# Kernel tuning notes

Hardware: AMD Instinct MI355X
Metric: run time of the kernel (lower is better)

Reference implementation:

```python
import jax, jax.numpy as jnp
import numpy as np

N_NODES = 50000
N_EDGES = 600000
N_GRAPHS = 1024
H = 128
VOCAB = 32
NC = 2
BN_EPS = 1e-5


def setup_inputs() -> dict:
    key = jax.random.key(0)
    ks = jax.random.split(key, 16)
    rn = lambda k, s, sc=0.05: jax.random.normal(k, s, jnp.float32) * sc
    inp = {}
    inp["node_feat"] = jax.random.randint(ks[0], (N_NODES,), 0, VOCAB, dtype=jnp.int32)
    inp["edge_src"] = jax.random.randint(ks[1], (N_EDGES,), 0, N_NODES, dtype=jnp.int32)
    inp["edge_dst"] = jax.random.randint(ks[2], (N_EDGES,), 0, N_NODES, dtype=jnp.int32)
    inp["graph_ids"] = jnp.sort(jax.random.randint(ks[3], (N_NODES,), 0, N_GRAPHS, dtype=jnp.int32))
    inp["emb"] = rn(ks[4], (VOCAB, H))
    inp["W1"] = rn(ks[5], (H, H)); inp["b1"] = jnp.zeros((H,), jnp.float32)
    inp["W2"] = rn(ks[6], (H, H)); inp["b2"] = jnp.zeros((H,), jnp.float32)
    inp["e1_w"] = rn(ks[7], (H, H));   inp["e1_b"] = jnp.zeros((H,), jnp.float32)
    inp["e2_w"] = rn(ks[8], (H, H));   inp["e2_b"] = jnp.zeros((H,), jnp.float32)
    inp["e3_w"] = rn(ks[9], (H, 64));  inp["e3_b"] = jnp.zeros((64,), jnp.float32)
    inp["e4_w"] = rn(ks[10], (64, 32)); inp["e4_b"] = jnp.zeros((32,), jnp.float32)
    inp["e5_w"] = rn(ks[11], (32, NC)); inp["e5_b"] = jnp.zeros((NC,), jnp.float32)
    inp["bn0_g"] = jnp.ones((H,), jnp.float32); inp["bn0_b"] = jnp.zeros((H,), jnp.float32)
    inp["bn1_g"] = jnp.ones((H,), jnp.float32); inp["bn1_b"] = jnp.zeros((H,), jnp.float32)
    return inp


def reference(node_feat, edge_src, edge_dst, graph_ids,
              emb, W1, b1, W2, b2,
              e1_w, e1_b, e2_w, e2_b, e3_w, e3_b, e4_w, e4_b, e5_w, e5_b,
              bn0_g, bn0_b, bn1_g, bn1_b):
    ones_e = jnp.ones((N_EDGES,), jnp.float32)
    out_deg = jax.ops.segment_sum(ones_e, edge_src, num_segments=N_NODES)
    in_deg = jax.ops.segment_sum(ones_e, edge_dst, num_segments=N_NODES)
    # DGL GraphConv norm='both': D_out^{-1/2} pre-scale, D_in^{-1/2} post-scale (deg clamped to 1)
    oi = jax.lax.rsqrt(jnp.maximum(out_deg, 1.0))  # [N]
    ii = jax.lax.rsqrt(jnp.maximum(in_deg, 1.0))   # [N]

    def gconv(h, W, b):
        m = (h * oi[:, None])[edge_src]                                   # [E,H] gather
        agg = jax.ops.segment_sum(m, edge_dst, num_segments=N_NODES)      # [N,H] scatter-add
        return (agg * ii[:, None]) @ W + b

    h = emb[node_feat]                       # [N,H] embedding lookup
    h = jax.nn.relu(gconv(h, W1, b1))
    h = jax.nn.relu(gconv(h, W2, b2))

    # dgl.mean_nodes: per-graph mean over nodes
    cnt = jax.ops.segment_sum(jnp.ones((N_NODES,), jnp.float32), graph_ids, num_segments=N_GRAPHS)
    hg = jax.ops.segment_sum(h, graph_ids, num_segments=N_GRAPHS) / jnp.maximum(cnt, 1.0)[:, None]

    def bn(x, g, b):  # BatchNorm1d, training-mode batch stats (biased var)
        mu = x.mean(0)
        var = x.var(0)
        return (x - mu) * jax.lax.rsqrt(var + BN_EPS) * g + b

    def lrelu(x, s):
        return jnp.where(x >= 0, x, s * x)

    h1 = lrelu(bn(hg @ e1_w + e1_b, bn0_g, bn0_b), 0.05)
    h2 = lrelu(bn(h1 @ e2_w + e2_b, bn1_g, bn1_b), 0.05)
    h3 = lrelu(h2 @ e3_w + e3_b, 0.1)
    h4 = lrelu(h3 @ e4_w + e4_b, 0.1)
    y = h4 @ e5_w + e5_b                      # [G, NC]
    return jax.nn.log_softmax(y, axis=1)
```

## Files before the change

kernel.cpp:

```cpp
#include <hip/hip_runtime.h>
#include <hip/hip_bf16.h>
#include <math.h>

#define N_NODES 50000
#define N_PAD   50048
#define N_EDGES 600000
#define N_GRAPHS 1024
#define H 128
#define VOCAB 32
#define BN_EPS 1e-5f
#define SCAN_BLOCKS ((N_NODES + 255) / 256)
#define H1_NODES 64
#define EB ((N_EDGES + 255) / 256)

typedef short bf8_t __attribute__((ext_vector_type(8)));
typedef float f4_t __attribute__((ext_vector_type(4)));

__global__ void k_count_prep(const int* __restrict__ src, int* __restrict__ cntO,
                             const float* __restrict__ emb, const float* __restrict__ W1,
                             float* __restrict__ emb1,
                             const float* __restrict__ W2, __hip_bfloat16* __restrict__ w2t) {
    int b = blockIdx.x;
    int t = threadIdx.x;
    if (b < EB) {
        int i = b * 256 + t;
        if (i < N_EDGES) atomicAdd(&cntO[src[i]], 1);
    } else if (b < EB + 32) {
        if (t < 128) {
            int v = b - EB;
            float acc = 0.f;
            for (int k = 0; k < H; ++k) acc += emb[v * H + k] * W1[k * H + t];
            emb1[v * H + t] = acc;
        }
    } else {
        if (t < 128) {
            int k = b - EB - 32;
            w2t[(size_t)t * H + k] = __float2bfloat16(W2[(size_t)k * H + t]);
        }
    }
}

__global__ void k_hist64(const int* __restrict__ src, const int* __restrict__ dst,
                         const int* __restrict__ feat, const int* __restrict__ cntO,
                         unsigned long long* __restrict__ wc,
                         unsigned char* __restrict__ rank8, int E) {
    int i = blockIdx.x * blockDim.x + threadIdx.x;
    if (i >= E) return;
    int s = src[i], d = dst[i], v = feat[s];
    float o = rsqrtf(fmaxf((float)cntO[s], 1.f));
    unsigned long long q = (unsigned long long)__float2uint_rn(o * 16777216.0f);
    unsigned long long old = atomicAdd(&wc[(size_t)d * VOCAB + v], (1ULL << 40) | q);
    rank8[i] = (unsigned char)(old >> 40);
}

__global__ void k_nodebins(const unsigned long long* __restrict__ wc,
                           int* __restrict__ cntI, unsigned char* __restrict__ binbase,
                           int* __restrict__ bsum, int n) {
    __shared__ int scnt[256];
    int t = threadIdx.x;
    int wave = t >> 6, lane = t & 63;
    int sub = lane >> 5;
    int l32 = lane & 31;
    int nodeBase = blockIdx.x * 256;
#pragma unroll 4
    for (int it = 0; it < 32; ++it) {
        int local = wave * 64 + it * 2 + sub;
        int node = nodeBase + local;
        int c = 0;
        if (node < n && l32 < VOCAB)
            c = (int)(wc[(size_t)node * VOCAB + l32] >> 40);
        int inc = c;
#pragma unroll
        for (int off = 1; off < VOCAB; off <<= 1) {
            int u = __shfl_up(inc, off, 32);
            if (l32 >= off) inc += u;
        }
        if (node < n && l32 < VOCAB)
            binbase[(size_t)node * VOCAB + l32] = (unsigned char)(inc - c);
        if (l32 == VOCAB - 1) scnt[local] = (node < n) ? inc : 0;
    }
    __syncthreads();
    int node = nodeBase + t;
    if (node < n) cntI[node] = scnt[t];
    __shared__ int red[256];
    red[t] = scnt[t];
    __syncthreads();
    for (int off = 128; off > 0; off >>= 1) {
        if (t < off) red[t] += red[t + off];
        __syncthreads();
    }
    if (t == 0) bsum[blockIdx.x] = red[0];
}

__global__ void k_scanbsum(int* __restrict__ bsum, int* __restrict__ row_ptr_last, int nb) {
    __shared__ int sh[256];
    int t = threadIdx.x;
    int v = (t < nb) ? bsum[t] : 0;
    sh[t] = v;
    __syncthreads();
    for (int off = 1; off < 256; off <<= 1) {
        int u = (t >= off) ? sh[t - off] : 0;
        __syncthreads();
        sh[t] += u;
        __syncthreads();
    }
    if (t < nb) bsum[t] = sh[t] - v;
    if (t == nb - 1) *row_ptr_last = sh[t];
}

__global__ void k_scatterscan(const int* __restrict__ cntI, const int* __restrict__ bsum,
                              int* __restrict__ row_ptr, float* __restrict__ ii, int n) {
    __shared__ int sh[256];
    int i = blockIdx.x * 256 + threadIdx.x;
    int t = threadIdx.x;
    int v = (i < n) ? cntI[i] : 0;
    sh[t] = v;
    __syncthreads();
    for (int off = 1; off < 256; off <<= 1) {
        int u = (t >= off) ? sh[t - off] : 0;
        __syncthreads();
        sh[t] += u;
        __syncthreads();
    }
    if (i < n) {
        row_ptr[i] = bsum[blockIdx.x] + sh[t] - v;
        ii[i] = rsqrtf(fmaxf((float)v, 1.f));
    }
}

#define H1_BLOCKS ((N_NODES + H1_NODES - 1) / H1_NODES)
__global__ void k_fill_h1(const int* __restrict__ src, const int* __restrict__ dst,
                          const int* __restrict__ feat, const int* __restrict__ row_ptr,
                          const unsigned char* __restrict__ binbase,
                          const unsigned char* __restrict__ rank8,
                          int* __restrict__ col,
                          const unsigned long long* __restrict__ wc,
                          const float* __restrict__ emb1,
                          const float* __restrict__ ii, const int* __restrict__ cntO,
                          const float* __restrict__ b1, __hip_bfloat16* __restrict__ h1) {
    __shared__ float wl[H1_NODES * VOCAB];
    __shared__ float sii[H1_NODES], soi[H1_NODES];
    int tid = threadIdx.x;
    if (blockIdx.x < EB) {
        int i = blockIdx.x * 256 + tid;
        if (i < N_EDGES) {
            int s = src[i], d = dst[i], v = feat[s];
            int slot = row_ptr[d] + (int)binbase[(size_t)d * VOCAB + v] + (int)rank8[i];
            col[slot] = s;
        }
        return;
    }
    int hb = blockIdx.x - EB;
    int j = tid & 127;
    int g = tid >> 7;
    float ev[VOCAB];
#pragma unroll
    for (int v = 0; v < VOCAB; ++v) ev[v] = emb1[v * H + j];
    float bj = b1[j];

    int node0 = hb * H1_NODES;
    int nn = min(H1_NODES, N_NODES - node0);
    const unsigned long long* wsrc = wc + (size_t)node0 * VOCAB;
    for (int i = tid; i < nn * VOCAB; i += 256) {
        unsigned long long p = wsrc[i];
        float lo = (float)((unsigned)p & 0xFFFFFFu);
        float hi = (float)((unsigned)(p >> 24) & 0xFFFFu);
        wl[i] = fmaf(lo, 1.0f / 16777216.0f, hi);
    }
    for (int i = tid; i < nn; i += 256) {
        sii[i] = ii[node0 + i];
        soi[i] = rsqrtf(fmaxf((float)cntO[node0 + i], 1.f));
    }
    __syncthreads();

    int rbeg = g * 32;
    int rend = min(rbeg + 32, nn);
    for (int r = rbeg; r < rend; ++r) {
        const float4* wr = (const float4*)(wl + r * VOCAB);
        float acc = 0.f;
#pragma unroll
        for (int q = 0; q < VOCAB / 4; ++q) {
            float4 w4 = wr[q];
            acc += w4.x * ev[4 * q] + w4.y * ev[4 * q + 1]
                 + w4.z * ev[4 * q + 2] + w4.w * ev[4 * q + 3];
        }
        float val = fmaxf(acc * sii[r] + bj, 0.f);
        h1[(size_t)(node0 + r) * H + j] = __float2bfloat16(val * soi[r]);
    }
}

__global__ void k_gather_bf(const __hip_bfloat16* __restrict__ h,
                            const int* __restrict__ row_ptr, const int* __restrict__ col,
                            __hip_bfloat16* __restrict__ out, int n) {
    int gid = blockIdx.x * blockDim.x + threadIdx.x;
    int wid = gid >> 6;
    int lane = gid & 63;
    int node = wid * 2 + (lane >> 5);
    int l32 = lane & 31;
    if (node >= n) return;
    int beg = row_ptr[node];
    int end = row_ptr[node + 1];
    int co = l32 * 4;
    float a0 = 0.f, a1 = 0.f, a2 = 0.f, a3 = 0.f;
    int e = beg;
    for (; e + 8 <= end; e += 8) {
#pragma unroll
        for (int k = 0; k < 8; ++k) {
            int s = col[e + k];
            uint2 v = *(const uint2*)(h + (size_t)s * H + co);
            float2 f0 = __bfloat1622float2(*(__hip_bfloat162*)&v.x);
            float2 f1 = __bfloat1622float2(*(__hip_bfloat162*)&v.y);
            a0 += f0.x; a1 += f0.y; a2 += f1.x; a3 += f1.y;
        }
    }
    for (; e < end; ++e) {
        int s = col[e];
        uint2 v = *(const uint2*)(h + (size_t)s * H + co);
        float2 f0 = __bfloat1622float2(*(__hip_bfloat162*)&v.x);
        float2 f1 = __bfloat1622float2(*(__hip_bfloat162*)&v.y);
        a0 += f0.x; a1 += f0.y; a2 += f1.x; a3 += f1.y;
    }
    __hip_bfloat162 o0 = __float22bfloat162_rn(make_float2(a0, a1));
    __hip_bfloat162 o1 = __float22bfloat162_rn(make_float2(a2, a3));
    uint2 ov;
    ov.x = *(unsigned*)&o0;
    ov.y = *(unsigned*)&o1;
    *(uint2*)(out + (size_t)node * H + co) = ov;
}

__global__ void k_transform_mfma(const __hip_bfloat16* __restrict__ A,
                                 const __hip_bfloat16* __restrict__ WT,
                                 const float* __restrict__ ii,
                                 const float* __restrict__ b,
                                 float* __restrict__ outp, int n) {
    int wave = threadIdx.x >> 6;
    int lane = threadIdx.x & 63;
    int row0 = blockIdx.x * 64 + wave * 16;
    int rl = lane & 15;
    int kg = lane >> 4;
    f4_t acc[8];
#pragma unroll
    for (int t = 0; t < 8; ++t) acc[t] = f4_t{0.f, 0.f, 0.f, 0.f};
    const __hip_bfloat16* arow = A + (size_t)(row0 + rl) * H + kg * 8;
#pragma unroll
    for (int ks = 0; ks < 4; ++ks) {
        bf8_t a = *(const bf8_t*)(arow + ks * 32);
#pragma unroll
        for (int t = 0; t < 8; ++t) {
            bf8_t bf = *(const bf8_t*)(WT + (size_t)(t * 16 + rl) * H + ks * 32 + kg * 8);
            acc[t] = __builtin_amdgcn_mfma_f32_16x16x32_bf16(a, bf, acc[t], 0, 0, 0);
        }
    }
    int rbase = row0 + kg * 4;
#pragma unroll
    for (int r = 0; r < 4; ++r) {
        int node = rbase + r;
        if (node < n) {
            float s = ii[node];
#pragma unroll
            for (int t = 0; t < 8; ++t) {
                int c = t * 16 + rl;
                float v = acc[t][r] * s + b[c];
                outp[(size_t)node * H + c] = fmaxf(v, 0.f);
            }
        }
    }
}

__global__ void k_poolmlp1(const float* __restrict__ h, const int* __restrict__ gid,
                           const float* __restrict__ e1w, const float* __restrict__ e1b,
                           float* __restrict__ t1, int n) {
    __shared__ int bnd[2];
    __shared__ float row[128];
    int g = blockIdx.x, t = threadIdx.x;
    if (t == 0) {
        int lo = 0, hi = n;
        while (lo < hi) { int m = (lo + hi) >> 1; if (gid[m] < g) lo = m + 1; else hi = m; }
        bnd[0] = lo;
        int lo2 = lo, hi2 = n;
        while (lo2 < hi2) { int m = (lo2 + hi2) >> 1; if (gid[m] < g + 1) lo2 = m + 1; else hi2 = m; }
        bnd[1] = lo2;
    }
    __syncthreads();
    int beg = bnd[0], end = bnd[1];
    float s = 0.f;
    for (int i = beg; i < end; ++i) s += h[(size_t)i * H + t];
    row[t] = s / fmaxf((float)(end - beg), 1.f);
    __syncthreads();
    float acc = e1b[t];
    for (int k = 0; k < H; ++k) acc += row[k] * e1w[k * H + t];
    t1[g * H + t] = acc;
}

__global__ void k_bnstat(const float* __restrict__ x, float* __restrict__ stats, int G) {
    int c = blockIdx.x;
    float s = 0.f, s2 = 0.f;
    for (int g = threadIdx.x; g < G; g += blockDim.x) {
        float v = x[g * H + c];
        s += v; s2 += v * v;
    }
    __shared__ float rs[256], rs2[256];
    rs[threadIdx.x] = s; rs2[threadIdx.x] = s2;
    __syncthreads();
    for (int off = 128; off > 0; off >>= 1) {
        if (threadIdx.x < off) { rs[threadIdx.x] += rs[threadIdx.x + off]; rs2[threadIdx.x] += rs2[threadIdx.x + off]; }
        __syncthreads();
    }
    if (threadIdx.x == 0) {
        float mu = rs[0] / G;
        stats[c] = mu;
        stats[H + c] = rs2[0] / G - mu * mu;
    }
}

__global__ void k_mlp2bn(const float* __restrict__ t1, const float* __restrict__ stats,
                         const float* __restrict__ gam, const float* __restrict__ bet,
                         const float* __restrict__ W, const float* __restrict__ bias,
                         float* __restrict__ t2) {
    __shared__ float x[128];
    int g = blockIdx.x, t = threadIdx.x;
    float v = t1[g * H + t];
    v = (v - stats[t]) * rsqrtf(stats[H + t] + BN_EPS) * gam[t] + bet[t];
    x[t] = (v >= 0.f) ? v : 0.05f * v;
    __syncthreads();
    float acc = bias[t];
    for (int k = 0; k < H; ++k) acc += x[k] * W[k * H + t];
    t2[g * H + t] = acc;
}

__global__ void k_head(const float* __restrict__ t2, const float* __restrict__ stats,
                       const float* __restrict__ gam, const float* __restrict__ bet,
                       const float* __restrict__ e3w, const float* __restrict__ e3b,
                       const float* __restrict__ e4w, const float* __restrict__ e4b,
                       const float* __restrict__ e5w, const float* __restrict__ e5b,
                       float* __restrict__ out) {
    __shared__ float x[128], h3[64], h4[32];
    int g = blockIdx.x, t = threadIdx.x;
    float v = t2[g * H + t];
    v = (v - stats[t]) * rsqrtf(stats[H + t] + BN_EPS) * gam[t] + bet[t];
    x[t] = (v >= 0.f) ? v : 0.05f * v;
    __syncthreads();
    if (t < 64) {
        float a = e3b[t];
        for (int k = 0; k < 128; ++k) a += x[k] * e3w[k * 64 + t];
        h3[t] = (a >= 0.f) ? a : 0.1f * a;
    }
    __syncthreads();
    if (t < 32) {
        float a = e4b[t];
        for (int k = 0; k < 64; ++k) a += h3[k] * e4w[k * 32 + t];
        h4[t] = (a >= 0.f) ? a : 0.1f * a;
    }
    __syncthreads();
    if (t == 0) {
        float y0 = e5b[0], y1 = e5b[1];
        for (int k = 0; k < 32; ++k) {
            y0 += h4[k] * e5w[2 * k];
            y1 += h4[k] * e5w[2 * k + 1];
        }
        float m = fmaxf(y0, y1);
        float l = m + logf(expf(y0 - m) + expf(y1 - m));
        out[2 * g] = y0 - l;
        out[2 * g + 1] = y1 - l;
    }
}

extern "C" void kernel_launch(void* const* d_in, const int* in_sizes, int n_in,
                              void* d_out, int out_size, void* d_ws, size_t ws_size,
                              hipStream_t stream) {
    const int*   node_feat = (const int*)d_in[0];
    const int*   edge_src  = (const int*)d_in[1];
    const int*   edge_dst  = (const int*)d_in[2];
    const int*   graph_ids = (const int*)d_in[3];
    const float* emb  = (const float*)d_in[4];
    const float* W1   = (const float*)d_in[5];
    const float* b1   = (const float*)d_in[6];
    const float* W2   = (const float*)d_in[7];
    const float* b2   = (const float*)d_in[8];
    const float* e1_w = (const float*)d_in[9];
    const float* e1_b = (const float*)d_in[10];
    const float* e2_w = (const float*)d_in[11];
    const float* e2_b = (const float*)d_in[12];
    const float* e3_w = (const float*)d_in[13];
    const float* e3_b = (const float*)d_in[14];
    const float* e4_w = (const float*)d_in[15];
    const float* e4_b = (const float*)d_in[16];
    const float* e5_w = (const float*)d_in[17];
    const float* e5_b = (const float*)d_in[18];
    const float* bn0_g = (const float*)d_in[19];
    const float* bn0_b = (const float*)d_in[20];
    const float* bn1_g = (const float*)d_in[21];
    const float* bn1_b = (const float*)d_in[22];
    float* out = (float*)d_out;

    float* ws = (float*)d_ws;
    float* bufA = ws;
    __hip_bfloat16* h1bf = (__hip_bfloat16*)(bufA + (size_t)N_NODES * H);
    __hip_bfloat16* aggbf = h1bf + (size_t)N_NODES * H;
    int*   cntO = (int*)(aggbf + (size_t)N_PAD * H);
    unsigned long long* wc = (unsigned long long*)(cntO + N_NODES);
    float* ii   = (float*)(wc + (size_t)N_NODES * VOCAB);
    int*   cntI = (int*)(ii + N_NODES);
    int*   row_ptr = cntI + N_NODES;
    int*   col  = row_ptr + 50048;
    unsigned char* binbase = (unsigned char*)(col + N_EDGES);
    unsigned char* rank8   = binbase + (size_t)N_NODES * VOCAB;
    float* t1   = (float*)(rank8 + ((N_EDGES + 63) & ~63));
    float* t2   = t1 + N_GRAPHS * H;
    float* stats = t2 + N_GRAPHS * H;
    int*   bsum  = (int*)(stats + 4 * H);
    float* emb1  = (float*)(bsum + 256);
    __hip_bfloat16* w2t = (__hip_bfloat16*)(emb1 + VOCAB * H);

    hipMemsetAsync(cntO, 0, N_NODES * sizeof(int) + (size_t)N_NODES * VOCAB * 8, stream);

    k_count_prep<<<EB + 160, 256, 0, stream>>>(edge_src, cntO, emb, W1, emb1, W2, w2t);
    k_hist64<<<EB, 256, 0, stream>>>(edge_src, edge_dst, node_feat, cntO, wc, rank8, N_EDGES);
    k_nodebins<<<SCAN_BLOCKS, 256, 0, stream>>>(wc, cntI, binbase, bsum, N_NODES);
    k_scanbsum<<<1, 256, 0, stream>>>(bsum, row_ptr + N_NODES, SCAN_BLOCKS);
    k_scatterscan<<<SCAN_BLOCKS, 256, 0, stream>>>(cntI, bsum, row_ptr, ii, N_NODES);
    k_fill_h1<<<EB + H1_BLOCKS, 256, 0, stream>>>(edge_src, edge_dst, node_feat, row_ptr,
                                                  binbase, rank8, col,
                                                  wc, emb1, ii, cntO, b1, h1bf);

    const int gb = ((N_NODES + 1) / 2 * 64 + 255) / 256;
    k_gather_bf<<<gb, 256, 0, stream>>>(h1bf, row_ptr, col, aggbf, N_NODES);
    k_transform_mfma<<<(N_NODES + 63) / 64, 256, 0, stream>>>(aggbf, w2t, ii, b2, bufA, N_NODES);

    k_poolmlp1<<<N_GRAPHS, 128, 0, stream>>>(bufA, graph_ids, e1_w, e1_b, t1, N_NODES);
    k_bnstat<<<H, 256, 0, stream>>>(t1, stats, N_GRAPHS);
    k_mlp2bn<<<N_GRAPHS, 128, 0, stream>>>(t1, stats, bn0_g, bn0_b, e2_w, e2_b, t2);
    k_bnstat<<<H, 256, 0, stream>>>(t2, stats + 2 * H, N_GRAPHS);
    k_head<<<N_GRAPHS, 128, 0, stream>>>(t2, stats + 2 * H, bn1_g, bn1_b,
                                         e3_w, e3_b, e4_w, e4_b, e5_w, e5_b, out);
}
```

Measured before the change: 220.6 us.

## Merge edge histogram into count kernel, compute layer-1 via CSR gather

The separate 64-bit weighted histogram kernel is dropped. Per-(dst,vocab) counts now use 32-bit atomics inside the out-degree counting kernel, and the two-level scan is folded into one kernel so a launch is saved. Layer-1 aggregation is now a per-node CSR gather over emb1 rows instead of a histogram-times-embedding product, and the layer-2 gather uses 16 lanes per node with 16-byte loads. In exchange, layer 1 now does a full per-edge gather with indirect feat/cntO loads instead of a 32-wide dot product, and it runs one small block per node, which may cost more than the histogram path.

```diff
diff --git a/kernel.cpp b/kernel.cpp
--- a/kernel.cpp
+++ b/kernel.cpp
@@ -10,21 +10,28 @@
 #define VOCAB 32
 #define BN_EPS 1e-5f
 #define SCAN_BLOCKS ((N_NODES + 255) / 256)
-#define H1_NODES 64
 #define EB ((N_EDGES + 255) / 256)
 
 typedef short bf8_t __attribute__((ext_vector_type(8)));
 typedef float f4_t __attribute__((ext_vector_type(4)));
 
-__global__ void k_count_prep(const int* __restrict__ src, int* __restrict__ cntO,
-                             const float* __restrict__ emb, const float* __restrict__ W1,
-                             float* __restrict__ emb1,
-                             const float* __restrict__ W2, __hip_bfloat16* __restrict__ w2t) {
+__global__ void k_edge(const int* __restrict__ src, const int* __restrict__ dst,
+                       const int* __restrict__ feat,
+                       int* __restrict__ cntO, unsigned* __restrict__ cnt32,
+                       unsigned char* __restrict__ rank8,
+                       const float* __restrict__ emb, const float* __restrict__ W1,
+                       float* __restrict__ emb1,
+                       const float* __restrict__ W2, __hip_bfloat16* __restrict__ w2t) {
     int b = blockIdx.x;
     int t = threadIdx.x;
     if (b < EB) {
         int i = b * 256 + t;
-        if (i < N_EDGES) atomicAdd(&cntO[src[i]], 1);
+        if (i < N_EDGES) {
+            int s = src[i];
+            atomicAdd(&cntO[s], 1);
+            unsigned old = atomicAdd(&cnt32[(size_t)dst[i] * VOCAB + feat[s]], 1u);
+            rank8[i] = (unsigned char)old;
+        }
     } else if (b < EB + 32) {
         if (t < 128) {
             int v = b - EB;
@@ -40,20 +47,7 @@
     }
 }
 
-__global__ void k_hist64(const int* __restrict__ src, const int* __restrict__ dst,
-                         const int* __restrict__ feat, const int* __restrict__ cntO,
-                         unsigned long long* __restrict__ wc,
-                         unsigned char* __restrict__ rank8, int E) {
-    int i = blockIdx.x * blockDim.x + threadIdx.x;
-    if (i >= E) return;
-    int s = src[i], d = dst[i], v = feat[s];
-    float o = rsqrtf(fmaxf((float)cntO[s], 1.f));
-    unsigned long long q = (unsigned long long)__float2uint_rn(o * 16777216.0f);
-    unsigned long long old = atomicAdd(&wc[(size_t)d * VOCAB + v], (1ULL << 40) | q);
-    rank8[i] = (unsigned char)(old >> 40);
-}
-
-__global__ void k_nodebins(const unsigned long long* __restrict__ wc,
+__global__ void k_nodebins(const unsigned* __restrict__ cnt32,
                            int* __restrict__ cntI, unsigned char* __restrict__ binbase,
                            int* __restrict__ bsum, int n) {
     __shared__ int scnt[256];
@@ -68,7 +62,7 @@
         int node = nodeBase + local;
         int c = 0;
         if (node < n && l32 < VOCAB)
-            c = (int)(wc[(size_t)node * VOCAB + l32] >> 40);
+            c = (int)cnt32[(size_t)node * VOCAB + l32];
         int inc = c;
 #pragma unroll
         for (int off = 1; off < VOCAB; off <<= 1) {
@@ -92,10 +86,24 @@
     if (t == 0) bsum[blockIdx.x] = red[0];
 }
 
-__global__ void k_scanbsum(int* __restrict__ bsum, int* __restrict__ row_ptr_last, int nb) {
+__global__ void k_scatterscan(const int* __restrict__ cntI, const int* __restrict__ bsum,
+                              int* __restrict__ row_ptr, float* __restrict__ ii,
+                              int n, int nb) {
+    __shared__ int sb[256];
     __shared__ int sh[256];
     int t = threadIdx.x;
-    int v = (t < nb) ? bsum[t] : 0;
+    int bv = (t < nb) ? bsum[t] : 0;
+    sb[t] = bv;
+    __syncthreads();
+    for (int off = 1; off < 256; off <<= 1) {
+        int u = (t >= off) ? sb[t - off] : 0;
+        __syncthreads();
+        sb[t] += u;
+        __syncthreads();
+    }
+    int blockoff = (blockIdx.x == 0) ? 0 : sb[blockIdx.x - 1];
+    int i = blockIdx.x * 256 + t;
+    int v = (i < n) ? cntI[i] : 0;
     sh[t] = v;
     __syncthreads();
     for (int off = 1; off < 256; off <<= 1) {
@@ -104,89 +112,42 @@
         sh[t] += u;
         __syncthreads();
     }
-    if (t < nb) bsum[t] = sh[t] - v;
-    if (t == nb - 1) *row_ptr_last = sh[t];
-}
-
-__global__ void k_scatterscan(const int* __restrict__ cntI, const int* __restrict__ bsum,
-                              int* __restrict__ row_ptr, float* __restrict__ ii, int n) {
-    __shared__ int sh[256];
-    int i = blockIdx.x * 256 + threadIdx.x;
-    int t = threadIdx.x;
-    int v = (i < n) ? cntI[i] : 0;
-    sh[t] = v;
-    __syncthreads();
-    for (int off = 1; off < 256; off <<= 1) {
-        int u = (t >= off) ? sh[t - off] : 0;
-        __syncthreads();
-        sh[t] += u;
-        __syncthreads();
-    }
     if (i < n) {
-        row_ptr[i] = bsum[blockIdx.x] + sh[t] - v;
+        row_ptr[i] = blockoff + sh[t] - v;
         ii[i] = rsqrtf(fmaxf((float)v, 1.f));
     }
-}
-
-#define H1_BLOCKS ((N_NODES + H1_NODES - 1) / H1_NODES)
-__global__ void k_fill_h1(const int* __restrict__ src, const int* __restrict__ dst,
-                          const int* __restrict__ feat, const int* __restrict__ row_ptr,
-                          const unsigned char* __restrict__ binbase,
-                          const unsigned char* __restrict__ rank8,
-                          int* __restrict__ col,
-                          const unsigned long long* __restrict__ wc,
-                          const float* __restrict__ emb1,
-                          const float* __restrict__ ii, const int* __restrict__ cntO,
-                          const float* __restrict__ b1, __hip_bfloat16* __restrict__ h1) {
-    __shared__ float wl[H1_NODES * VOCAB];
-    __shared__ float sii[H1_NODES], soi[H1_NODES];
-    int tid = threadIdx.x;
-    if (blockIdx.x < EB) {
-        int i = blockIdx.x * 256 + tid;
-        if (i < N_EDGES) {
-            int s = src[i], d = dst[i], v = feat[s];
-            int slot = row_ptr[d] + (int)binbase[(size_t)d * VOCAB + v] + (int)rank8[i];
-            col[slot] = s;
-        }
-        return;
-    }
-    int hb = blockIdx.x - EB;
-    int j = tid & 127;
-    int g = tid >> 7;
-    float ev[VOCAB];
-#pragma unroll
-    for (int v = 0; v < VOCAB; ++v) ev[v] = emb1[v * H + j];
-    float bj = b1[j];
-
-    int node0 = hb * H1_NODES;
-    int nn = min(H1_NODES, N_NODES - node0);
-    const unsigned long long* wsrc = wc + (size_t)node0 * VOCAB;
-    for (int i = tid; i < nn * VOCAB; i += 256) {
-        unsigned long long p = wsrc[i];
-        float lo = (float)((unsigned)p & 0xFFFFFFu);
-        float hi = (float)((unsigned)(p >> 24) & 0xFFFFu);
-        wl[i] = fmaf(lo, 1.0f / 16777216.0f, hi);
-    }
-    for (int i = tid; i < nn; i += 256) {
-        sii[i] = ii[node0 + i];
-        soi[i] = rsqrtf(fmaxf((float)cntO[node0 + i], 1.f));
-    }
-    __syncthreads();
-
-    int rbeg = g * 32;
-    int rend = min(rbeg + 32, nn);
-    for (int r = rbeg; r < rend; ++r) {
-        const float4* wr = (const float4*)(wl + r * VOCAB);
-        float acc = 0.f;
-#pragma unroll
-        for (int q = 0; q < VOCAB / 4; ++q) {
-            float4 w4 = wr[q];
-            acc += w4.x * ev[4 * q] + w4.y * ev[4 * q + 1]
-                 + w4.z * ev[4 * q + 2] + w4.w * ev[4 * q + 3];
-        }
-        float val = fmaxf(acc * sii[r] + bj, 0.f);
-        h1[(size_t)(node0 + r) * H + j] = __float2bfloat16(val * soi[r]);
-    }
+    if (blockIdx.x == 0 && t == 0) row_ptr[n] = sb[nb - 1];
+}
+
+__global__ void k_fill(const int* __restrict__ src, const int* __restrict__ dst,
+                       const int* __restrict__ feat, const int* __restrict__ row_ptr,
+                       const unsigned char* __restrict__ binbase,
+                       const unsigned char* __restrict__ rank8,
+                       int* __restrict__ col, int E) {
+    int i = blockIdx.x * blockDim.x + threadIdx.x;
+    if (i >= E) return;
+    int s = src[i], d = dst[i], v = feat[s];
+    int slot = row_ptr[d] + (int)binbase[(size_t)d * VOCAB + v] + (int)rank8[i];
+    col[slot] = s;
+}
+
+__global__ void k_h1(const int* __restrict__ row_ptr, const int* __restrict__ col,
+                     const int* __restrict__ feat, const int* __restrict__ cntO,
+                     const float* __restrict__ emb1, const float* __restrict__ ii,
+                     const float* __restrict__ b1, __hip_bfloat16* __restrict__ h1) {
+    int node = blockIdx.x;
+    int j = threadIdx.x;
+    int beg = row_ptr[node];
+    int end = row_ptr[node + 1];
+    float acc = 0.f;
+    for (int e = beg; e < end; ++e) {
+        int s = col[e];
+        float o = rsqrtf(fmaxf((float)cntO[s], 1.f));
+        acc += o * emb1[feat[s] * H + j];
+    }
+    float val = fmaxf(acc * ii[node] + b1[j], 0.f);
+    float onode = rsqrtf(fmaxf((float)cntO[node], 1.f));
+    h1[(size_t)node * H + j] = __float2bfloat16(val * onode);
 }
 
 __global__ void k_gather_bf(const __hip_bfloat16* __restrict__ h,
@@ -195,37 +156,46 @@
     int gid = blockIdx.x * blockDim.x + threadIdx.x;
     int wid = gid >> 6;
     int lane = gid & 63;
-    int node = wid * 2 + (lane >> 5);
-    int l32 = lane & 31;
+    int node = wid * 4 + (lane >> 4);
+    int l16 = lane & 15;
     if (node >= n) return;
     int beg = row_ptr[node];
     int end = row_ptr[node + 1];
-    int co = l32 * 4;
+    int co = l16 * 8;
     float a0 = 0.f, a1 = 0.f, a2 = 0.f, a3 = 0.f;
+    float a4 = 0.f, a5 = 0.f, a6 = 0.f, a7 = 0.f;
     int e = beg;
     for (; e + 8 <= end; e += 8) {
 #pragma unroll
         for (int k = 0; k < 8; ++k) {
             int s = col[e + k];
-            uint2 v = *(const uint2*)(h + (size_t)s * H + co);
+            uint4 v = *(const uint4*)(h + (size_t)s * H + co);
             float2 f0 = __bfloat1622float2(*(__hip_bfloat162*)&v.x);
             float2 f1 = __bfloat1622float2(*(__hip_bfloat162*)&v.y);
+            float2 f2 = __bfloat1622float2(*(__hip_bfloat162*)&v.z);
+            float2 f3 = __bfloat1622float2(*(__hip_bfloat162*)&v.w);
             a0 += f0.x; a1 += f0.y; a2 += f1.x; a3 += f1.y;
+            a4 += f2.x; a5 += f2.y; a6 += f3.x; a7 += f3.y;
         }
     }
     for (; e < end; ++e) {
         int s = col[e];
-        uint2 v = *(const uint2*)(h + (size_t)s * H + co);
+        uint4 v = *(const uint4*)(h + (size_t)s * H + co);
         float2 f0 = __bfloat1622float2(*(__hip_bfloat162*)&v.x);
         float2 f1 = __bfloat1622float2(*(__hip_bfloat162*)&v.y);
+        float2 f2 = __bfloat1622float2(*(__hip_bfloat162*)&v.z);
+        float2 f3 = __bfloat1622float2(*(__hip_bfloat162*)&v.w);
         a0 += f0.x; a1 += f0.y; a2 += f1.x; a3 += f1.y;
+        a4 += f2.x; a5 += f2.y; a6 += f3.x; a7 += f3.y;
     }
     __hip_bfloat162 o0 = __float22bfloat162_rn(make_float2(a0, a1));
     __hip_bfloat162 o1 = __float22bfloat162_rn(make_float2(a2, a3));
-    uint2 ov;
-    ov.x = *(unsigned*)&o0;
-    ov.y = *(unsigned*)&o1;
-    *(uint2*)(out + (size_t)node * H + co) = ov;
+    __hip_bfloat162 o2 = __float22bfloat162_rn(make_float2(a4, a5));
+    __hip_bfloat162 o3 = __float22bfloat162_rn(make_float2(a6, a7));
+    uint4 ov;
+    ov.x = *(unsigned*)&o0; ov.y = *(unsigned*)&o1;
+    ov.z = *(unsigned*)&o2; ov.w = *(unsigned*)&o3;
+    *(uint4*)(out + (size_t)node * H + co) = ov;
 }
 
 __global__ void k_transform_mfma(const __hip_bfloat16* __restrict__ A,
@@ -398,8 +368,8 @@
     __hip_bfloat16* h1bf = (__hip_bfloat16*)(bufA + (size_t)N_NODES * H);
     __hip_bfloat16* aggbf = h1bf + (size_t)N_NODES * H;
     int*   cntO = (int*)(aggbf + (size_t)N_PAD * H);
-    unsigned long long* wc = (unsigned long long*)(cntO + N_NODES);
-    float* ii   = (float*)(wc + (size_t)N_NODES * VOCAB);
+    unsigned* cnt32 = (unsigned*)(cntO + N_NODES);
+    float* ii   = (float*)(cnt32 + (size_t)N_NODES * VOCAB);
     int*   cntI = (int*)(ii + N_NODES);
     int*   row_ptr = cntI + N_NODES;
     int*   col  = row_ptr + 50048;
@@ -412,18 +382,18 @@
     float* emb1  = (float*)(bsum + 256);
     __hip_bfloat16* w2t = (__hip_bfloat16*)(emb1 + VOCAB * H);
 
-    hipMemsetAsync(cntO, 0, N_NODES * sizeof(int) + (size_t)N_NODES * VOCAB * 8, stream);
-
-    k_count_prep<<<EB + 160, 256, 0, stream>>>(edge_src, cntO, emb, W1, emb1, W2, w2t);
-    k_hist64<<<EB, 256, 0, stream>>>(edge_src, edge_dst, node_feat, cntO, wc, rank8, N_EDGES);
-    k_nodebins<<<SCAN_BLOCKS, 256, 0, stream>>>(wc, cntI, binbase, bsum, N_NODES);
-    k_scanbsum<<<1, 256, 0, stream>>>(bsum, row_ptr + N_NODES, SCAN_BLOCKS);
-    k_scatterscan<<<SCAN_BLOCKS, 256, 0, stream>>>(cntI, bsum, row_ptr, ii, N_NODES);
-    k_fill_h1<<<EB + H1_BLOCKS, 256, 0, stream>>>(edge_src, edge_dst, node_feat, row_ptr,
-                                                  binbase, rank8, col,
-                                                  wc, emb1, ii, cntO, b1, h1bf);
-
-    const int gb = ((N_NODES + 1) / 2 * 64 + 255) / 256;
+    hipMemsetAsync(cntO, 0, (N_NODES + N_NODES * VOCAB) * sizeof(int), stream);
+
+    k_edge<<<EB + 160, 256, 0, stream>>>(edge_src, edge_dst, node_feat, cntO, cnt32, rank8,
+                                         emb, W1, emb1, W2, w2t);
+    k_nodebins<<<SCAN_BLOCKS, 256, 0, stream>>>(cnt32, cntI, binbase, bsum, N_NODES);
+    k_scatterscan<<<SCAN_BLOCKS, 256, 0, stream>>>(cntI, bsum, row_ptr, ii, N_NODES, SCAN_BLOCKS);
+    k_fill<<<EB, 256, 0, stream>>>(edge_src, edge_dst, node_feat, row_ptr, binbase, rank8,
+                                   col, N_EDGES);
+
+    k_h1<<<N_NODES, 128, 0, stream>>>(row_ptr, col, node_feat, cntO, emb1, ii, b1, h1bf);
+
+    const int gb = (((N_NODES + 3) / 4) * 64 + 255) / 256;
     k_gather_bf<<<gb, 256, 0, stream>>>(h1bf, row_ptr, col, aggbf, N_NODES);
     k_transform_mfma<<<(N_NODES + 63) / 64, 256, 0, stream>>>(aggbf, w2t, ii, b2, bufA, N_NODES);
 
```

After: 267.8 us. 21.4% more time.
